# Performance work log

Measured on AMD Instinct MI355X. Metric: run time of the kernel, lower is better.

## Reference

```python
import jax, jax.numpy as jnp
import numpy as np

B, L, C_IN = 32, 1024, 21
D, H, DFF, MODES, LAYERS = 512, 8, 2048, 64, 2
E = D // H            # 64, matches FourierBlock weights1 [8, D//8, D//8, modes]
K_MA = 25             # moving_avg kernel
EPS = 1e-5

def _pos_encoding(n, d):
    pos = np.arange(n)[:, None].astype(np.float32)
    div = np.exp(np.arange(0, d, 2).astype(np.float32) * -(np.log(10000.0) / d))
    pe = np.zeros((n, d), np.float32)
    pe[:, 0::2] = np.sin(pos * div)
    pe[:, 1::2] = np.cos(pos * div)
    return jnp.asarray(pe)

PE = _pos_encoding(L, D)

def _moving_avg(x, k):
    # series_decomp: replicate-pad (k-1)//2 on both ends, then mean window k
    pad = (k - 1) // 2
    xp = jnp.pad(x, ((0, 0), (pad, pad), (0, 0)), mode='edge')
    return jax.lax.reduce_window(xp, 0.0, jax.lax.add, (1, k, 1), (1, 1, 1), 'VALID') / k

def _layernorm(x, g, b):
    mu = x.mean(-1, keepdims=True)
    var = ((x - mu) ** 2).mean(-1, keepdims=True)
    return (x - mu) * jax.lax.rsqrt(var + EPS) * g + b

def _fourier_block(q, w_cplx):
    # q: [B,L,H,E] -> [B,H,E,L]; keep only lowest MODES frequencies,
    # complex per-mode channel mixing, then inverse rFFT.
    x = q.transpose(0, 2, 3, 1)
    x_ft = jnp.fft.rfft(x, axis=-1)                          # [B,H,E,L//2+1] complex
    out_m = jnp.einsum('bhem,heom->bhom', x_ft[..., :MODES], w_cplx)
    out_ft = jnp.zeros(x_ft.shape[:3] + (L // 2 + 1,), jnp.complex64)
    out_ft = out_ft.at[..., :MODES].set(out_m)
    return jnp.fft.irfft(out_ft, n=L, axis=-1)               # [B,H,E,L] real

def _forward(x_enc, conv_w, wq, bq, wo, bo, fw_re, fw_im, conv1_w, conv2_w,
             enc_g, enc_b, ff_w, ff_b, ffn_g, ffn_b, reg_w, reg_b):
    # DataEmbedding_onlypos: circular Conv1d(k=3, no bias) + sinusoidal PE (dropout=0)
    xt = x_enc.transpose(0, 2, 1)                            # [B,C,L]
    xp = jnp.pad(xt, ((0, 0), (0, 0), (1, 1)), mode='wrap')
    emb = jax.lax.conv_general_dilated(xp, conv_w, (1,), 'VALID',
                                       dimension_numbers=('NCH', 'OIH', 'NCH'))
    x = emb.transpose(0, 2, 1) + PE                          # [B,L,D]
    for l in range(LAYERS):
        # AutoCorrelationLayer: only the query projection feeds FourierBlock
        q = (jnp.einsum('bld,kd->blk', x, wq[l]) + bq[l]).reshape(B, L, H, E)
        new_x = _fourier_block(q, fw_re[l] + 1j * fw_im[l])  # [B,H,E,L]
        # torch .view(B, L, -1) on contiguous [B,H,E,L] = raw reshape
        new_x = new_x.reshape(B, L, H * E)
        new_x = jnp.einsum('bld,kd->blk', new_x, wo[l]) + bo[l]
        x = x + new_x
        x = x - _moving_avg(x, K_MA)                         # decomp1 -> residual part
        y = jax.nn.gelu(jnp.einsum('bld,fd->blf', x, conv1_w[l]), approximate=False)
        y = jnp.einsum('blf,df->bld', y, conv2_w[l])
        xy = x + y
        x = xy - _moving_avg(xy, K_MA)                       # decomp2 -> residual part
    # my_Layernorm: LN then subtract per-sequence mean
    x = _layernorm(x, enc_g, enc_b)
    x = x - x.mean(axis=1, keepdims=True)
    x = _layernorm(jnp.einsum('bld,kd->blk', x, ff_w) + ff_b, ffn_g, ffn_b)
    flat = x.reshape(B, L * D)
    return flat @ reg_w.T + reg_b                            # [B,1]

def setup_inputs():
    key = jax.random.key(0)
    ks = jax.random.split(key, 12)
    r = lambda k, shp, s=0.02: jax.random.normal(k, shp, jnp.float32) * s
    scale = 1.0 / (D * D)
    return {
        'x_enc': jax.random.normal(ks[0], (B, L, C_IN), jnp.float32),
        'conv_w': r(ks[1], (D, C_IN, 3), 0.05),
        'wq': r(ks[2], (LAYERS, D, D)),
        'bq': jnp.zeros((LAYERS, D), jnp.float32),
        'wo': r(ks[3], (LAYERS, D, D)),
        'bo': jnp.zeros((LAYERS, D), jnp.float32),
        'fw_re': jax.random.uniform(ks[4], (LAYERS, H, E, E, MODES), jnp.float32) * scale,
        'fw_im': jax.random.uniform(ks[5], (LAYERS, H, E, E, MODES), jnp.float32) * scale,
        'conv1_w': r(ks[6], (LAYERS, DFF, D)),
        'conv2_w': r(ks[7], (LAYERS, D, DFF)),
        'enc_g': jnp.ones((D,), jnp.float32),
        'enc_b': jnp.zeros((D,), jnp.float32),
        'ff_w': r(ks[8], (D, D)),
        'ff_b': jnp.zeros((D,), jnp.float32),
        'ffn_g': jnp.ones((D,), jnp.float32),
        'ffn_b': jnp.zeros((D,), jnp.float32),
        'reg_w': r(ks[9], (1, D * L)),
        'reg_b': jnp.zeros((1,), jnp.float32),
    }

def reference(x_enc, conv_w, wq, bq, wo, bo, fw_re, fw_im, conv1_w, conv2_w,
              enc_g, enc_b, ff_w, ff_b, ffn_g, ffn_b, reg_w, reg_b):
    return _forward(x_enc, conv_w, wq, bq, wo, bo, fw_re, fw_im, conv1_w, conv2_w,
                    enc_g, enc_b, ff_w, ff_b, ffn_g, ffn_b, reg_w, reg_b)
```

## Files before the change

### kernel.cpp

```cpp
#include <hip/hip_runtime.h>
#include <math.h>

static constexpr int B_   = 32;
static constexpr int L_   = 1024;
static constexpr int CIN_ = 21;
static constexpr int D_   = 512;
static constexpr int H_   = 8;
static constexpr int E_   = 64;
static constexpr int DFF_ = 2048;
static constexpr int M_   = 64;

typedef unsigned short u16;
typedef __attribute__((ext_vector_type(8))) short bf16x8;
typedef __attribute__((ext_vector_type(4))) float f32x4;
typedef __attribute__((ext_vector_type(4))) unsigned short u16x4;

static __device__ __forceinline__ u16 f2b(float f) {
    unsigned u = __float_as_uint(f);
    unsigned r = (u + 0x7fffu + ((u >> 16) & 1u)) >> 16;
    return (u16)r;
}
static __device__ __forceinline__ float b2f(u16 x) {
    return __uint_as_float((unsigned)x << 16);
}

static __device__ __forceinline__ void gload16(const u16* g, u16* l) {
    unsigned long long ga = (unsigned long long)g;
    unsigned la = (unsigned)(unsigned long long)l;
    __builtin_amdgcn_global_load_lds(
        (const __attribute__((address_space(1))) void*)ga,
        (__attribute__((address_space(3))) void*)(unsigned long long)la,
        16, 0, 0);
}

__global__ void k_tables(u16* trig, u16* tcat, float* pe) {
    int idx = blockIdx.x * 256 + threadIdx.x;
    if (idx < 131072) {
        int l = idx & 1023, mc = idx >> 10;
        int m = mc & 63;
        float th = (float)((m * l) & 1023) * 0.006135923151542565f;
        float v = (mc < 64) ? cosf(th) : (-sinf(th));
        trig[idx] = f2b(v);
    }
    if (idx < 131072) {
        int k = idx & 127, l = idx >> 7;
        int m = k & 63;
        float th = (float)((m * l) & 1023) * 0.006135923151542565f;
        float v;
        if (k < 64) v = (m == 0) ? 1.0f : (2.0f * cosf(th));
        else        v = (m == 0) ? 0.0f : (-2.0f * sinf(th));
        tcat[idx] = f2b(v * (1.0f / 1024.0f));
    }
    if (idx < 524288) {
        int d = idx & 511, l = idx >> 9;
        int i2 = d >> 1;
        float div = expf(-(float)(2 * i2) * 0.017988946039015984f);
        float arg = (float)l * div;
        pe[idx] = (d & 1) ? cosf(arg) : sinf(arg);
    }
}

__global__ void k_cast(const float* __restrict__ in, u16* __restrict__ out, int n4) {
    int i = blockIdx.x * 256 + threadIdx.x;
    if (i < n4) {
        float4 v = ((const float4*)in)[i];
        u16x4 o = { f2b(v.x), f2b(v.y), f2b(v.z), f2b(v.w) };
        ((u16x4*)out)[i] = o;
    }
}

__global__ void k_wtrans(const float* __restrict__ re, const float* __restrict__ im,
                         u16* __restrict__ outre, u16* __restrict__ outim) {
    __shared__ float t[64][65];
    const float* src = blockIdx.z ? im : re;
    u16* dst = blockIdx.z ? outim : outre;
    int h = blockIdx.y, eo0 = blockIdx.x * 64;
    int j = threadIdx.x & 63, i0 = threadIdx.x >> 6;
    for (int i = i0; i < 64; i += 4)
        t[i][j] = src[(size_t)h * 262144 + (size_t)(eo0 + i) * 64 + j];
    __syncthreads();
    for (int i = i0; i < 64; i += 4)
        dst[(size_t)h * 262144 + (size_t)i * 4096 + eo0 + j] = f2b(t[j][i]);
}

__global__ __launch_bounds__(512) void k_embed(
        const float* __restrict__ xe, const float* __restrict__ cw,
        const float* __restrict__ pe, float* __restrict__ x32,
        u16* __restrict__ x16) {
    __shared__ float strip[34][21];
    int b = blockIdx.y, l0 = blockIdx.x * 32;
    int d = threadIdx.x;
    for (int i = d; i < 34 * 21; i += 512) {
        int r = i / 21, c = i - r * 21;
        int ls = (l0 + r - 1 + 1024) & 1023;
        strip[r][c] = xe[((size_t)b * 1024 + ls) * 21 + c];
    }
    __syncthreads();
    float w[3][21];
    #pragma unroll
    for (int k = 0; k < 3; ++k)
        #pragma unroll
        for (int c = 0; c < 21; ++c)
            w[k][c] = cw[(size_t)d * 63 + c * 3 + k];
    float a0[21], a1[21];
    #pragma unroll
    for (int c = 0; c < 21; ++c) { a0[c] = strip[0][c]; a1[c] = strip[1][c]; }
    for (int li = 0; li < 32; ++li) {
        float acc = 0.f;
        #pragma unroll
        for (int c = 0; c < 21; ++c) {
            float a2 = strip[li + 2][c];
            acc += w[0][c] * a0[c] + w[1][c] * a1[c] + w[2][c] * a2;
            a0[c] = a1[c]; a1[c] = a2;
        }
        int l = l0 + li;
        float v = acc + pe[(size_t)l * 512 + d];
        size_t o = ((size_t)b * 1024 + l) * 512 + d;
        x32[o] = v;
        x16[o] = f2b(v);
    }
}

template<bool BIAS, bool BIASR, bool GELU, bool ADD, bool WF32, bool WBF16,
         bool DFTZ = false>
__global__ __launch_bounds__(256, 3) void k_mfma(
        const u16* __restrict__ A, const u16* __restrict__ W,
        const float* __restrict__ bias, const float* addp,
        float* C32, u16* C16,
        int K, int lda, int ldw, int ldc, long strideA, long strideC) {
    __shared__ __align__(16) u16 As[128 * 32];
    __shared__ __align__(16) u16 Bs[128 * 32];
    const int tid  = threadIdx.x;
    const int lane = tid & 63, wid = tid >> 6;
    int m0, n0;
    size_t cbase;
    if constexpr (DFTZ) {
        int z  = blockIdx.z;
        int ks = z >> 5;
        m0 = 0;
        n0 = blockIdx.x * 128;
        A += (size_t)ks * 256;
        W += (size_t)(z & 31) * 1024 + (size_t)ks * 256;
        cbase = (size_t)z * 65536;
    } else {
        m0 = blockIdx.y * 128;
        n0 = blockIdx.x * 128;
        A += (size_t)blockIdx.z * strideA;
        cbase = (size_t)blockIdx.z * strideC;
    }

    const int srow = lane >> 2, scol = (lane & 3) * 8;
    const u16* ga0 = A + (size_t)(m0 + wid * 32 + srow) * lda + scol;
    const u16* ga1 = ga0 + (size_t)16 * lda;
    const u16* gb0 = W + (size_t)(n0 + wid * 32 + srow) * ldw + scol;
    const u16* gb1 = gb0 + (size_t)16 * ldw;
    u16* la0 = &As[wid * 32 * 32];
    u16* la1 = la0 + 16 * 32;
    u16* lb0 = &Bs[wid * 32 * 32];
    u16* lb1 = lb0 + 16 * 32;

    const int wr = wid >> 1, wc = wid & 1;
    const int fr = lane & 15, fg = lane >> 4;

    f32x4 acc[4][4];
    #pragma unroll
    for (int i = 0; i < 4; ++i)
        #pragma unroll
        for (int j = 0; j < 4; ++j)
            acc[i][j] = f32x4{0.f, 0.f, 0.f, 0.f};

    for (int k0 = 0; k0 < K; k0 += 32) {
        __syncthreads();
        gload16(ga0 + k0, la0);
        gload16(ga1 + k0, la1);
        gload16(gb0 + k0, lb0);
        gload16(gb1 + k0, lb1);
        __syncthreads();
        bf16x8 af[4], bfr[4];
        #pragma unroll
        for (int i = 0; i < 4; ++i) {
            af[i]  = *(const bf16x8*)&As[(wr * 64 + i * 16 + fr) * 32 + fg * 8];
            bfr[i] = *(const bf16x8*)&Bs[(wc * 64 + i * 16 + fr) * 32 + fg * 8];
        }
        #pragma unroll
        for (int i = 0; i < 4; ++i)
            #pragma unroll
            for (int j = 0; j < 4; ++j)
                acc[i][j] = __builtin_amdgcn_mfma_f32_16x16x32_bf16(
                    af[i], bfr[j], acc[i][j], 0, 0, 0);
    }

    #pragma unroll
    for (int i = 0; i < 4; ++i) {
        #pragma unroll
        for (int j = 0; j < 4; ++j) {
            #pragma unroll
            for (int r = 0; r < 4; ++r) {
                int row = m0 + wr * 64 + i * 16 + fg * 4 + r;
                int col = n0 + wc * 64 + j * 16 + fr;
                float v = acc[i][j][r];
                if (BIAS)  v += bias[col];
                if (BIASR) v += bias[row];
                if (GELU) v = 0.5f * v * (1.f + erff(v * 0.70710678118f));
                size_t o = cbase + (size_t)row * ldc + col;
                if (ADD)  v += addp[o];
                if (WF32) C32[o] = v;
                if (WBF16) C16[o] = f2b(v);
            }
        }
    }
}

__global__ void k_modemix(const float* __restrict__ ftT,
                          const u16* __restrict__ wtre, const u16* __restrict__ wtim,
                          u16* __restrict__ acat) {
    __shared__ float wr_s[64][64];
    __shared__ float wi_s[64][64];
    __shared__ float fr_s[32][64];
    __shared__ float fi_s[32][64];
    int h = blockIdx.x >> 6, m = blockIdx.x & 63;
    int tid = threadIdx.x;
    const u16* wr_p = wtre + ((size_t)(h * 64 + m)) * 4096;
    const u16* wi_p = wtim + ((size_t)(h * 64 + m)) * 4096;
    for (int i = tid; i < 4096; i += 256) {
        wr_s[i >> 6][i & 63] = b2f(wr_p[i]);
        wi_s[i >> 6][i & 63] = b2f(wi_p[i]);
    }
    const size_t KS = (size_t)32 * 65536;
    for (int i = tid; i < 2048; i += 256) {
        int b = i >> 6, e = i & 63;
        size_t f0 = (size_t)b * 65536 + (size_t)m * 512 + h * 64 + e;
        size_t f1 = f0 + (size_t)64 * 512;
        fr_s[b][e] = ftT[f0] + ftT[f0 + KS] + ftT[f0 + 2 * KS] + ftT[f0 + 3 * KS];
        fi_s[b][e] = ftT[f1] + ftT[f1 + KS] + ftT[f1 + 2 * KS] + ftT[f1 + 3 * KS];
    }
    __syncthreads();
    int o = tid & 63, bg = tid >> 6;
    for (int bb = bg; bb < 32; bb += 4) {
        float accr = 0.f, acci = 0.f;
        #pragma unroll 8
        for (int e = 0; e < 64; ++e) {
            float wr = wr_s[e][o], wi = wi_s[e][o];
            float fr = fr_s[bb][e], fi = fi_s[bb][e];
            accr += fr * wr - fi * wi;
            acci += fr * wi + fi * wr;
        }
        size_t base = (((size_t)(bb * 8 + h)) * 64 + o) * 128;
        acat[base + m]      = f2b(accr);
        acat[base + 64 + m] = f2b(acci);
    }
}

__global__ void k_madiff(const float* __restrict__ in, float* __restrict__ out,
                         u16* __restrict__ out16) {
    int b = blockIdx.x, ls = blockIdx.y;
    int d2 = threadIdx.x;
    const float2* base = (const float2*)(in + (size_t)b * 524288) + d2;
    int l0 = ls * 64;
    float sx = 0.f, sy = 0.f;
    #pragma unroll
    for (int k = -12; k <= 12; ++k) {
        int ll = l0 + k;
        ll = ll < 0 ? 0 : (ll > 1023 ? 1023 : ll);
        float2 v = base[(size_t)ll * 256];
        sx += v.x; sy += v.y;
    }
    for (int li = 0; li < 64; ++li) {
        int l = l0 + li;
        float2 x = base[(size_t)l * 256];
        float vx = x.x - sx * (1.f / 25.f);
        float vy = x.y - sy * (1.f / 25.f);
        size_t o = (size_t)b * 262144 + (size_t)l * 256 + d2;
        ((float2*)out)[o] = float2{vx, vy};
        unsigned pk = (unsigned)f2b(vx) | ((unsigned)f2b(vy) << 16);
        ((unsigned*)out16)[o] = pk;
        int lp = l + 13; lp = lp > 1023 ? 1023 : lp;
        int lm = l - 12; lm = lm < 0 ? 0 : lm;
        float2 a = base[(size_t)lp * 256];
        float2 s = base[(size_t)lm * 256];
        sx += a.x - s.x; sy += a.y - s.y;
    }
}

__global__ void k_layernorm(const float* __restrict__ in, const float* __restrict__ g,
                            const float* __restrict__ bta, float* __restrict__ out) {
    int row = blockIdx.x;
    int tid = threadIdx.x;
    const float* r = in + (size_t)row * 512;
    float v0 = r[tid], v1 = r[tid + 256];
    float s = v0 + v1, s2 = v0 * v0 + v1 * v1;
    #pragma unroll
    for (int off = 32; off; off >>= 1) {
        s  += __shfl_down(s, off);
        s2 += __shfl_down(s2, off);
    }
    __shared__ float ws[4], ws2[4];
    if ((tid & 63) == 0) { ws[tid >> 6] = s; ws2[tid >> 6] = s2; }
    __syncthreads();
    if (tid == 0) {
        ws[0]  = ws[0] + ws[1] + ws[2] + ws[3];
        ws2[0] = ws2[0] + ws2[1] + ws2[2] + ws2[3];
    }
    __syncthreads();
    float mu = ws[0] * (1.f / 512.f);
    float var = ws2[0] * (1.f / 512.f) - mu * mu;
    float rs = rsqrtf(var + 1e-5f);
    float* o = out + (size_t)row * 512;
    o[tid]       = (v0 - mu) * rs * g[tid]       + bta[tid];
    o[tid + 256] = (v1 - mu) * rs * g[tid + 256] + bta[tid + 256];
}

__global__ void k_lnreg(const float* __restrict__ in, const float* __restrict__ g,
                        const float* __restrict__ bta, const float* __restrict__ rw,
                        float* __restrict__ partial) {
    int row = blockIdx.x;
    int tid = threadIdx.x;
    const float* r = in + (size_t)row * 512;
    float v0 = r[tid], v1 = r[tid + 256];
    float s = v0 + v1, s2 = v0 * v0 + v1 * v1;
    #pragma unroll
    for (int off = 32; off; off >>= 1) {
        s  += __shfl_down(s, off);
        s2 += __shfl_down(s2, off);
    }
    __shared__ float ws[4], ws2[4];
    if ((tid & 63) == 0) { ws[tid >> 6] = s; ws2[tid >> 6] = s2; }
    __syncthreads();
    if (tid == 0) {
        ws[0]  = ws[0] + ws[1] + ws[2] + ws[3];
        ws2[0] = ws2[0] + ws2[1] + ws2[2] + ws2[3];
    }
    __syncthreads();
    float mu = ws[0] * (1.f / 512.f);
    float var = ws2[0] * (1.f / 512.f) - mu * mu;
    float rs = rsqrtf(var + 1e-5f);
    const float* wrow = rw + (size_t)(row & 1023) * 512;
    float y0 = (v0 - mu) * rs * g[tid]       + bta[tid];
    float y1 = (v1 - mu) * rs * g[tid + 256] + bta[tid + 256];
    float p = y0 * wrow[tid] + y1 * wrow[tid + 256];
    #pragma unroll
    for (int off = 32; off; off >>= 1) p += __shfl_down(p, off);
    __shared__ float wp[4];
    if ((tid & 63) == 0) wp[tid >> 6] = p;
    __syncthreads();
    if (tid == 0) partial[row] = wp[0] + wp[1] + wp[2] + wp[3];
}

__global__ void k_regf2(const float* __restrict__ partial, const float* __restrict__ rb,
                        float* __restrict__ out) {
    int b = blockIdx.x;
    int tid = threadIdx.x;
    const float* p = partial + (size_t)b * 1024;
    float s = p[tid] + p[tid + 256] + p[tid + 512] + p[tid + 768];
    #pragma unroll
    for (int off = 32; off; off >>= 1) s += __shfl_down(s, off);
    __shared__ float ws[4];
    if ((tid & 63) == 0) ws[tid >> 6] = s;
    __syncthreads();
    if (tid == 0) out[b] = ws[0] + ws[1] + ws[2] + ws[3] + rb[0];
}

__global__ __launch_bounds__(512) void k_colmean1(const float* __restrict__ in,
                                                  float* __restrict__ part) {
    int b = blockIdx.x, seg = blockIdx.y;
    int d = threadIdx.x;
    const float* p = in + ((size_t)b * 1024 + seg * 128) * 512 + d;
    float s = 0.f;
    for (int l = 0; l < 128; ++l) s += p[(size_t)l * 512];
    part[((size_t)b * 8 + seg) * 512 + d] = s;
}

__global__ void k_colmean2(const float* __restrict__ part, float* __restrict__ mean) {
    int i = blockIdx.x * 256 + threadIdx.x;
    int b = i >> 9, d = i & 511;
    float s = 0.f;
    #pragma unroll
    for (int seg = 0; seg < 8; ++seg) s += part[((size_t)b * 8 + seg) * 512 + d];
    mean[i] = s * (1.f / 1024.f);
}

__global__ void k_subcol(float* __restrict__ x, const float* __restrict__ mean,
                         u16* __restrict__ x16) {
    int idx = blockIdx.x * 256 + threadIdx.x;
    int d = idx & 511;
    int b = idx >> 19;
    float v = x[idx] - mean[b * 512 + d];
    x[idx] = v;
    x16[idx] = f2b(v);
}

extern "C" void kernel_launch(void* const* d_in, const int* in_sizes, int n_in,
                              void* d_out, int out_size, void* d_ws, size_t ws_size,
                              hipStream_t stream) {
    const float* x_enc  = (const float*)d_in[0];
    const float* conv_w = (const float*)d_in[1];
    const float* wq     = (const float*)d_in[2];
    const float* bq     = (const float*)d_in[3];
    const float* wo     = (const float*)d_in[4];
    const float* bo     = (const float*)d_in[5];
    const float* fw_re  = (const float*)d_in[6];
    const float* fw_im  = (const float*)d_in[7];
    const float* c1w    = (const float*)d_in[8];
    const float* c2w    = (const float*)d_in[9];
    const float* enc_g  = (const float*)d_in[10];
    const float* enc_b  = (const float*)d_in[11];
    const float* ff_w   = (const float*)d_in[12];
    const float* ff_b   = (const float*)d_in[13];
    const float* ffn_g  = (const float*)d_in[14];
    const float* ffn_b  = (const float*)d_in[15];
    const float* reg_w  = (const float*)d_in[16];
    const float* reg_b  = (const float*)d_in[17];
    float* out = (float*)d_out;

    char* wsb = (char*)d_ws;
    float* F0    = (float*)(wsb);
    float* F1    = (float*)(wsb + 67108864);
    u16*   A16   = (u16*)  (wsb + 134217728);
    u16*   U16   = (u16*)  (wsb + 167772160);
    u16*   AC16  = (u16*)  (wsb + 201326592);
    float* FTT   = (float*)(wsb + 205520896);
    float* PE    = (float*)(wsb + 213909504);
    u16*   TRIG  = (u16*)  (wsb + 216006656);
    u16*   TCAT  = (u16*)  (wsb + 216268800);
    u16*   WQ16  = (u16*)  (wsb + 216530944);
    u16*   WO16  = (u16*)  (wsb + 217579520);
    u16*   C1W16 = (u16*)  (wsb + 218628096);
    u16*   C2W16 = (u16*)  (wsb + 222822400);
    u16*   FFW16 = (u16*)  (wsb + 227016704);
    float* CMEAN = (float*)(wsb + 227540992);
    const size_t need_bytes = 227606528;
    if (ws_size < need_bytes) return;

    u16* WTRE16 = (u16*)FTT;
    u16* WTIM16 = WTRE16 + 2097152;

    const int BLD = B_ * L_ * D_;
    dim3 blk(256);

    k_tables<<<2048, blk, 0, stream>>>(TRIG, TCAT, PE);
    k_cast<<<512,  blk, 0, stream>>>(wq,   WQ16,  524288 / 4);
    k_cast<<<512,  blk, 0, stream>>>(wo,   WO16,  524288 / 4);
    k_cast<<<2048, blk, 0, stream>>>(c1w,  C1W16, 2097152 / 4);
    k_cast<<<2048, blk, 0, stream>>>(c2w,  C2W16, 2097152 / 4);
    k_cast<<<256,  blk, 0, stream>>>(ff_w, FFW16, 262144 / 4);
    k_embed<<<dim3(32, 32), 512, 0, stream>>>(x_enc, conv_w, PE, F0, A16);

    float* cur = F0;
    float* alt = F1;
    const dim3 g_big(4, 256);

    for (int l = 0; l < 2; ++l) {
        const float* bq_l = bq + l * 512;
        const float* bo_l = bo + l * 512;
        const u16* wo16_l = WO16 + (size_t)l * 262144;
        const u16* c1_l   = C1W16 + (size_t)l * DFF_ * D_;
        const u16* c2_l   = C2W16 + (size_t)l * D_ * DFF_;
        const float* fwre_l = fw_re + (size_t)l * H_ * E_ * E_ * M_;
        const float* fwim_l = fw_im + (size_t)l * H_ * E_ * E_ * M_;

        k_wtrans<<<dim3(64, 8, 2), blk, 0, stream>>>(fwre_l, fwim_l, WTRE16, WTIM16);
        k_mfma<false, true, false, false, false, true><<<dim3(256, 4), blk, 0, stream>>>(
            WQ16 + (size_t)l * 262144, A16, bq_l, nullptr, nullptr, U16,
            512, 512, 512, 32768, 0, 0);
        float* ftt4 = alt;
        k_mfma<false, false, false, false, true, false, true>
            <<<dim3(4, 1, 128), blk, 0, stream>>>(
            TRIG, U16, nullptr, nullptr, ftt4, nullptr,
            256, 1024, 32768, 512, 0, 0);
        k_modemix<<<512, blk, 0, stream>>>(ftt4, WTRE16, WTIM16, AC16);
        k_mfma<false, false, false, false, false, true><<<dim3(8, 128), blk, 0, stream>>>(
            AC16, TCAT, nullptr, nullptr, nullptr, U16, 128, 128, 128, 1024, 0, 0);
        k_mfma<true, false, false, true, true, false><<<g_big, blk, 0, stream>>>(
            U16, wo16_l, bo_l, cur, cur, nullptr, 512, 512, 512, 512, 0, 0);
        k_madiff<<<dim3(32, 16), blk, 0, stream>>>(cur, alt, A16);
        { float* t = cur; cur = alt; alt = t; }
        u16* y16 = (u16*)alt;
        for (int c = 0; c < 2; ++c) {
            const size_t aoff = (size_t)c * 16384 * 512;
            k_mfma<false, false, true, false, false, true><<<dim3(16, 128), blk, 0, stream>>>(
                A16 + aoff, c1_l, nullptr, nullptr, nullptr, y16,
                512, 512, 512, 2048, 0, 0);
            k_mfma<false, false, false, true, true, false><<<dim3(4, 128), blk, 0, stream>>>(
                y16, c2_l, nullptr, cur + aoff, cur + aoff, nullptr,
                2048, 2048, 2048, 512, 0, 0);
        }
        k_madiff<<<dim3(32, 16), blk, 0, stream>>>(cur, alt, A16);
        { float* t = cur; cur = alt; alt = t; }
    }

    k_layernorm<<<32768, blk, 0, stream>>>(cur, enc_g, enc_b, alt);
    k_colmean1<<<dim3(B_, 8), 512, 0, stream>>>(alt, FTT);
    k_colmean2<<<64, blk, 0, stream>>>(FTT, CMEAN);
    k_subcol<<<BLD / 256, blk, 0, stream>>>(alt, CMEAN, A16);
    k_mfma<true, false, false, false, true, false><<<g_big, blk, 0, stream>>>(
        A16, FFW16, ff_b, nullptr, cur, nullptr, 512, 512, 512, 512, 0, 0);
    k_lnreg<<<32768, blk, 0, stream>>>(cur, ffn_g, ffn_b, reg_w, FTT);
    k_regf2<<<32, blk, 0, stream>>>(FTT, reg_b, out);
}
```

Baseline: 1.189 ms.

## Convert embedding conv to im2col MFMA GEMM and double GEMM K-step per sync

Replaces the scalar circular Conv1d embedding with an im2col pass plus a bf16 MFMA GEMM whose epilogue adds the positional encoding. The general GEMM kernel now loads two 32-wide K slices into separate LDS buffers per barrier pair, halving synchronization rounds. This doubles LDS usage per block, which may reduce occupancy. It also computes the embedding in bf16 instead of fp32.

```diff
diff --git a/kernel.cpp b/kernel.cpp
--- a/kernel.cpp
+++ b/kernel.cpp
@@ -83,53 +83,43 @@
         dst[(size_t)h * 262144 + (size_t)i * 4096 + eo0 + j] = f2b(t[j][i]);
 }
 
-__global__ __launch_bounds__(512) void k_embed(
-        const float* __restrict__ xe, const float* __restrict__ cw,
-        const float* __restrict__ pe, float* __restrict__ x32,
-        u16* __restrict__ x16) {
-    __shared__ float strip[34][21];
-    int b = blockIdx.y, l0 = blockIdx.x * 32;
-    int d = threadIdx.x;
-    for (int i = d; i < 34 * 21; i += 512) {
-        int r = i / 21, c = i - r * 21;
-        int ls = (l0 + r - 1 + 1024) & 1023;
-        strip[r][c] = xe[((size_t)b * 1024 + ls) * 21 + c];
-    }
-    __syncthreads();
-    float w[3][21];
-    #pragma unroll
-    for (int k = 0; k < 3; ++k)
-        #pragma unroll
-        for (int c = 0; c < 21; ++c)
-            w[k][c] = cw[(size_t)d * 63 + c * 3 + k];
-    float a0[21], a1[21];
-    #pragma unroll
-    for (int c = 0; c < 21; ++c) { a0[c] = strip[0][c]; a1[c] = strip[1][c]; }
-    for (int li = 0; li < 32; ++li) {
-        float acc = 0.f;
-        #pragma unroll
-        for (int c = 0; c < 21; ++c) {
-            float a2 = strip[li + 2][c];
-            acc += w[0][c] * a0[c] + w[1][c] * a1[c] + w[2][c] * a2;
-            a0[c] = a1[c]; a1[c] = a2;
+__global__ void k_im2col(const float* __restrict__ xe, u16* __restrict__ a2) {
+    int idx = blockIdx.x * 256 + threadIdx.x;
+    int row = idx >> 4, g = idx & 15;
+    int b = row >> 10, l = row & 1023;
+    u16x4 o;
+    #pragma unroll
+    for (int j = 0; j < 4; ++j) {
+        int kc = g * 4 + j;
+        float v = 0.f;
+        if (kc < 63) {
+            int c = kc / 3, k = kc - c * 3;
+            int ls = (l + k - 1 + 1024) & 1023;
+            v = xe[((size_t)b * 1024 + ls) * 21 + c];
         }
-        int l = l0 + li;
-        float v = acc + pe[(size_t)l * 512 + d];
-        size_t o = ((size_t)b * 1024 + l) * 512 + d;
-        x32[o] = v;
-        x16[o] = f2b(v);
-    }
+        o[j] = f2b(v);
+    }
+    *(u16x4*)(a2 + (size_t)row * 64 + g * 4) = o;
+}
+
+__global__ void k_wpad(const float* __restrict__ cw, u16* __restrict__ w2) {
+    int idx = blockIdx.x * 256 + threadIdx.x;
+    int d = idx >> 6, kc = idx & 63;
+    float v = (kc < 63) ? cw[(size_t)d * 63 + kc] : 0.f;
+    w2[idx] = f2b(v);
 }
 
 template<bool BIAS, bool BIASR, bool GELU, bool ADD, bool WF32, bool WBF16,
-         bool DFTZ = false>
+         bool DFTZ = false, bool PEADD = false>
 __global__ __launch_bounds__(256, 3) void k_mfma(
         const u16* __restrict__ A, const u16* __restrict__ W,
         const float* __restrict__ bias, const float* addp,
         float* C32, u16* C16,
         int K, int lda, int ldw, int ldc, long strideA, long strideC) {
-    __shared__ __align__(16) u16 As[128 * 32];
-    __shared__ __align__(16) u16 Bs[128 * 32];
+    __shared__ __align__(16) u16 As0[128 * 32];
+    __shared__ __align__(16) u16 As1[128 * 32];
+    __shared__ __align__(16) u16 Bs0[128 * 32];
+    __shared__ __align__(16) u16 Bs1[128 * 32];
     const int tid  = threadIdx.x;
     const int lane = tid & 63, wid = tid >> 6;
     int m0, n0;
@@ -154,10 +144,7 @@
     const u16* ga1 = ga0 + (size_t)16 * lda;
     const u16* gb0 = W + (size_t)(n0 + wid * 32 + srow) * ldw + scol;
     const u16* gb1 = gb0 + (size_t)16 * ldw;
-    u16* la0 = &As[wid * 32 * 32];
-    u16* la1 = la0 + 16 * 32;
-    u16* lb0 = &Bs[wid * 32 * 32];
-    u16* lb1 = lb0 + 16 * 32;
+    const int lofs0 = wid * 32 * 32, lofs1 = lofs0 + 16 * 32;
 
     const int wr = wid >> 1, wc = wid & 1;
     const int fr = lane & 15, fg = lane >> 4;
@@ -169,25 +156,45 @@
         for (int j = 0; j < 4; ++j)
             acc[i][j] = f32x4{0.f, 0.f, 0.f, 0.f};
 
-    for (int k0 = 0; k0 < K; k0 += 32) {
+    for (int k0 = 0; k0 < K; k0 += 64) {
         __syncthreads();
-        gload16(ga0 + k0, la0);
-        gload16(ga1 + k0, la1);
-        gload16(gb0 + k0, lb0);
-        gload16(gb1 + k0, lb1);
+        gload16(ga0 + k0,      &As0[lofs0]);
+        gload16(ga1 + k0,      &As0[lofs1]);
+        gload16(gb0 + k0,      &Bs0[lofs0]);
+        gload16(gb1 + k0,      &Bs0[lofs1]);
+        gload16(ga0 + k0 + 32, &As1[lofs0]);
+        gload16(ga1 + k0 + 32, &As1[lofs1]);
+        gload16(gb0 + k0 + 32, &Bs1[lofs0]);
+        gload16(gb1 + k0 + 32, &Bs1[lofs1]);
         __syncthreads();
-        bf16x8 af[4], bfr[4];
-        #pragma unroll
-        for (int i = 0; i < 4; ++i) {
-            af[i]  = *(const bf16x8*)&As[(wr * 64 + i * 16 + fr) * 32 + fg * 8];
-            bfr[i] = *(const bf16x8*)&Bs[(wc * 64 + i * 16 + fr) * 32 + fg * 8];
+        {
+            bf16x8 af[4], bfr[4];
+            #pragma unroll
+            for (int i = 0; i < 4; ++i) {
+                af[i]  = *(const bf16x8*)&As0[(wr * 64 + i * 16 + fr) * 32 + fg * 8];
+                bfr[i] = *(const bf16x8*)&Bs0[(wc * 64 + i * 16 + fr) * 32 + fg * 8];
+            }
+            #pragma unroll
+            for (int i = 0; i < 4; ++i)
+                #pragma unroll
+                for (int j = 0; j < 4; ++j)
+                    acc[i][j] = __builtin_amdgcn_mfma_f32_16x16x32_bf16(
+                        af[i], bfr[j], acc[i][j], 0, 0, 0);
         }
-        #pragma unroll
-        for (int i = 0; i < 4; ++i)
+        {
+            bf16x8 af[4], bfr[4];
             #pragma unroll
-            for (int j = 0; j < 4; ++j)
-                acc[i][j] = __builtin_amdgcn_mfma_f32_16x16x32_bf16(
-                    af[i], bfr[j], acc[i][j], 0, 0, 0);
+            for (int i = 0; i < 4; ++i) {
+                af[i]  = *(const bf16x8*)&As1[(wr * 64 + i * 16 + fr) * 32 + fg * 8];
+                bfr[i] = *(const bf16x8*)&Bs1[(wc * 64 + i * 16 + fr) * 32 + fg * 8];
+            }
+            #pragma unroll
+            for (int i = 0; i < 4; ++i)
+                #pragma unroll
+                for (int j = 0; j < 4; ++j)
+                    acc[i][j] = __builtin_amdgcn_mfma_f32_16x16x32_bf16(
+                        af[i], bfr[j], acc[i][j], 0, 0, 0);
+        }
     }
 
     #pragma unroll
@@ -203,7 +210,8 @@
                 if (BIASR) v += bias[row];
                 if (GELU) v = 0.5f * v * (1.f + erff(v * 0.70710678118f));
                 size_t o = cbase + (size_t)row * ldc + col;
-                if (ADD)  v += addp[o];
+                if (PEADD) v += addp[(size_t)(row & 1023) * 512 + col];
+                if (ADD)   v += addp[o];
                 if (WF32) C32[o] = v;
                 if (WBF16) C16[o] = f2b(v);
             }
@@ -443,7 +451,11 @@
     k_cast<<<2048, blk, 0, stream>>>(c1w,  C1W16, 2097152 / 4);
     k_cast<<<2048, blk, 0, stream>>>(c2w,  C2W16, 2097152 / 4);
     k_cast<<<256,  blk, 0, stream>>>(ff_w, FFW16, 262144 / 4);
-    k_embed<<<dim3(32, 32), 512, 0, stream>>>(x_enc, conv_w, PE, F0, A16);
+    k_wpad<<<128, blk, 0, stream>>>(conv_w, AC16);
+    k_im2col<<<2048, blk, 0, stream>>>(x_enc, U16);
+    k_mfma<false, false, false, false, true, true, false, true>
+        <<<dim3(4, 256), blk, 0, stream>>>(
+        U16, AC16, nullptr, PE, F0, A16, 64, 64, 64, 512, 0, 0);
 
     float* cur = F0;
     float* alt = F1;
```

New measurement: 1.096 ms. -7.8%, faster.
